# Kernel tuning notes

Measured on AMD Instinct MI355X. Metric: run time of the kernel, lower is better.

Reference implementation:

```python
import jax, jax.numpy as jnp
import numpy as np

C_IN = 128
C_INNER = 128


def setup_inputs() -> dict:
    key = jax.random.key(0)
    ks = jax.random.split(key, 9)
    b, c, h, w = 4, C_IN, 64, 64
    s = 1.0 / np.sqrt(c)
    x = jax.random.normal(ks[0], (b, c, h, w), dtype=jnp.float32)
    Wq = jax.random.normal(ks[1], (C_INNER, C_IN), dtype=jnp.float32) * s
    bq = jnp.zeros((C_INNER,), dtype=jnp.float32)
    Wk = jax.random.normal(ks[2], (C_INNER, C_IN), dtype=jnp.float32) * s
    bk = jnp.zeros((C_INNER,), dtype=jnp.float32)
    Wv = jax.random.normal(ks[3], (C_INNER, C_IN), dtype=jnp.float32) * s
    bv = jnp.zeros((C_INNER,), dtype=jnp.float32)
    Wo = jax.random.normal(ks[4], (C_IN, C_INNER), dtype=jnp.float32) * (1.0 / np.sqrt(C_INNER))
    bo = jnp.zeros((C_IN,), dtype=jnp.float32)
    return {"x": x, "Wq": Wq, "bq": bq, "Wk": Wk, "bk": bk,
            "Wv": Wv, "bv": bv, "Wo": Wo, "bo": bo}


def _conv1x1(x, W, bias):
    # x: (b,c,h,w), W: (o,c) -> (b,o,h,w)
    return jnp.einsum('oc,bchw->bohw', W, x) + bias[None, :, None, None]


def reference(x, Wq, bq, Wk, bk, Wv, bv, Wo, bo):
    b, c, h, w = x.shape
    ci = Wq.shape[0]
    n = h * w
    q = _conv1x1(x, Wq, bq).reshape(b, ci, n)          # (b, ci, n)
    k = _conv1x1(x, Wk, bk).reshape(b, ci, n)          # (b, ci, n)
    v = _conv1x1(x, Wv, bv).reshape(b, ci, n)          # (b, ci, n)
    # attn = softmax(q^T @ k) over keys
    attn = jnp.einsum('bci,bcj->bij', q, k)            # (b, n, n)
    attn = jax.nn.softmax(attn, axis=-1)
    out = jnp.einsum('bij,bcj->bci', attn, v)          # (b, ci, n)
    out = out.reshape(b, ci, h, w)
    out = _conv1x1(out, Wo, bo)
    return out + x
```

## Files before the change

### kernel.cpp

```cpp
#include <hip/hip_runtime.h>
#include <math.h>
#include <stdint.h>

#define CDIM 128
#define NTOT 4096

typedef _Float16 f16x8 __attribute__((ext_vector_type(8)));
typedef float floatx4 __attribute__((ext_vector_type(4)));

static __device__ __forceinline__ floatx4 mfma16(f16x8 a, f16x8 b, floatx4 c) {
    return __builtin_amdgcn_mfma_f32_16x16x32_f16(a, b, c, 0, 0, 0);
}
static __device__ __forceinline__ unsigned short f2h(float f) {
    _Float16 h = (_Float16)f;
    return __builtin_bit_cast(unsigned short, h);
}
static __device__ __forceinline__ float h2f(unsigned short u) {
    return (float)__builtin_bit_cast(_Float16, u);
}
static __device__ __forceinline__ f16x8 ldW8f(const float* p) {
    float4 a = *(const float4*)p;
    float4 c = *(const float4*)(p + 4);
    f16x8 r;
    r[0] = (_Float16)a.x; r[1] = (_Float16)a.y; r[2] = (_Float16)a.z; r[3] = (_Float16)a.w;
    r[4] = (_Float16)c.x; r[5] = (_Float16)c.y; r[6] = (_Float16)c.z; r[7] = (_Float16)c.w;
    return r;
}

#define SWZ(row, cc) ((((row) << 7)) + ((((cc) ^ ((row) & 15))) << 3))
#define SWZ8(row, cc) ((((row) << 6)) + ((((cc) ^ ((row) & 7))) << 3))

static __device__ __forceinline__ void gload_lds16(const void* g, void* l) {
    __builtin_amdgcn_global_load_lds(
        (const __attribute__((address_space(1))) void*)g,
        (__attribute__((address_space(3))) void*)l, 16, 0, 0);
}

__global__ __launch_bounds__(256) void qkv_proj_kernel(
    const float* __restrict__ x,
    const float* __restrict__ Wq, const float* __restrict__ Wk,
    const float* __restrict__ Wv,
    const float* __restrict__ bq, const float* __restrict__ bk,
    const float* __restrict__ bv,
    unsigned short* __restrict__ qo, unsigned short* __restrict__ ko,
    unsigned short* __restrict__ vo)
{
    __shared__ __align__(16) unsigned short Xs[16][136];

    const int t = threadIdx.x;
    const int bid = blockIdx.x;
    const int swz = ((bid & 7) << 7) | (bid >> 3);
    const int b = swz >> 8;
    const int n0 = (swz & 255) * 16;
    const int w = t >> 6, quad = (t >> 4) & 3, l15 = t & 15;

    {
        const int n = (t & 3) * 4;
        const int c = (t >> 2) * 2;
        float4 xr[2];
        #pragma unroll
        for (int j = 0; j < 2; ++j)
            xr[j] = *(const float4*)&x[((size_t)b * CDIM + c + j) * NTOT + n0 + n];
        #pragma unroll
        for (int k = 0; k < 4; ++k) {
            ushort2 u;
            u.x = f2h(((const float*)&xr[0])[k]);
            u.y = f2h(((const float*)&xr[1])[k]);
            *(ushort2*)&Xs[n + k][c] = u;
        }
    }
    __syncthreads();

    f16x8 xf[4];
    #pragma unroll
    for (int f = 0; f < 4; ++f)
        xf[f] = *(const f16x8*)&Xs[l15][f * 32 + quad * 8];

    #pragma unroll
    for (int s = 0; s < 2; ++s) {
        const float* Wm = s ? Wk : Wq;
        const float* bias = s ? bk : bq;
        unsigned short* dst = s ? ko : qo;
        #pragma unroll
        for (int ot = 0; ot < 2; ++ot) {
            const int o = w * 32 + ot * 16;
            floatx4 acc = (floatx4){0.f, 0.f, 0.f, 0.f};
            #pragma unroll
            for (int f = 0; f < 4; ++f) {
                f16x8 aW = ldW8f(&Wm[(size_t)(o + l15) * CDIM + f * 32 + quad * 8]);
                acc = mfma16(aW, xf[f], acc);
            }
            const int ob = o + quad * 4;
            ushort4 u;
            u.x = f2h(acc[0] + bias[ob + 0]);
            u.y = f2h(acc[1] + bias[ob + 1]);
            u.z = f2h(acc[2] + bias[ob + 2]);
            u.w = f2h(acc[3] + bias[ob + 3]);
            *(ushort4*)&dst[((size_t)b * NTOT + n0 + l15) * CDIM + ob] = u;
        }
    }
    {
        #pragma unroll
        for (int ot = 0; ot < 2; ++ot) {
            const int o = w * 32 + ot * 16 + l15;
            floatx4 acc = (floatx4){0.f, 0.f, 0.f, 0.f};
            #pragma unroll
            for (int f = 0; f < 4; ++f) {
                f16x8 bW = ldW8f(&Wv[(size_t)o * CDIM + f * 32 + quad * 8]);
                acc = mfma16(xf[f], bW, acc);
            }
            const float bv_ = bv[o];
            ushort4 u;
            u.x = f2h(acc[0] + bv_); u.y = f2h(acc[1] + bv_);
            u.z = f2h(acc[2] + bv_); u.w = f2h(acc[3] + bv_);
            *(ushort4*)&vo[((size_t)b * CDIM + o) * NTOT + n0 + quad * 4] = u;
        }
    }
}

__global__ __launch_bounds__(256, 2) void attn_kernel(
    const unsigned short* __restrict__ qg,
    const unsigned short* __restrict__ kg,
    const unsigned short* __restrict__ vg,
    unsigned short* __restrict__ Op,
    float* __restrict__ Ms, float* __restrict__ Ls)
{
    __shared__ __align__(16) unsigned short Kb[2][64 * 128];
    __shared__ __align__(16) unsigned short Vb[2][128 * 64];
    __shared__ __align__(16) unsigned short Ps[128 * 64];

    const int t = threadIdx.x;
    const int w = t >> 6, quad = (t >> 4) & 3, l15 = t & 15;

    const int bid = blockIdx.x;
    const int swz = ((bid & 7) << 6) | (bid >> 3);
    const int gidx = swz >> 5;
    const int b = gidx & 3;
    const int z = gidx >> 2;
    const int i0 = (swz & 31) * 128;
    const int jbase = z * 1024;
    const size_t vbase = (size_t)b * CDIM * NTOT;

    f16x8 bQ[2][4];
    #pragma unroll
    for (int nt = 0; nt < 2; ++nt) {
        const size_t qrow = ((size_t)b * NTOT + i0 + w * 32 + nt * 16 + l15) * CDIM;
        #pragma unroll
        for (int f = 0; f < 4; ++f)
            bQ[nt][f] = *(const f16x8*)&qg[qrow + f * 32 + quad * 8];
    }

    auto stageK = [&](unsigned short* Kd, int j0) {
        const size_t kbase = ((size_t)b * NTOT + j0) * CDIM;
        #pragma unroll
        for (int r = 0; r < 4; ++r) {
            const int flat = r * 256 + t;
            const int ldsoff = (r * 256 + (t & ~63)) * 8;
            const int krow = flat >> 4, kcc = flat & 15;
            gload_lds16(&kg[kbase + (size_t)krow * CDIM + ((kcc ^ (krow & 15)) << 3)],
                        &Kd[ldsoff]);
        }
    };
    auto stageV = [&](unsigned short* Vd, int j0) {
        const size_t vrow0 = vbase + j0;
        #pragma unroll
        for (int r = 0; r < 4; ++r) {
            const int flat = r * 256 + t;
            const int ldsoff = (r * 256 + (t & ~63)) * 8;
            const int vrow = flat >> 3, vcc = flat & 7;
            gload_lds16(&vg[vrow0 + (size_t)vrow * NTOT + ((vcc ^ (vrow & 7)) << 3)],
                        &Vd[ldsoff]);
        }
    };

    floatx4 accO[2][8];
    #pragma unroll
    for (int nt = 0; nt < 2; ++nt)
        #pragma unroll
        for (int dt = 0; dt < 8; ++dt) accO[nt][dt] = (floatx4){0.f, 0.f, 0.f, 0.f};
    float m_run[2] = {-INFINITY, -INFINITY};
    float l_part[2] = {0.f, 0.f};

    floatx4 accT[2][4];
    uint2 pu[2][4];
    f16x8 bP[2][2];

    auto QK = [&](const unsigned short* Kd) {
        #pragma unroll
        for (int nt = 0; nt < 2; ++nt)
            #pragma unroll
            for (int jt = 0; jt < 4; ++jt) accT[nt][jt] = (floatx4){0.f, 0.f, 0.f, 0.f};
        __builtin_amdgcn_s_setprio(1);
        #pragma unroll
        for (int jt = 0; jt < 4; ++jt)
            #pragma unroll
            for (int f = 0; f < 4; ++f) {
                f16x8 aK = *(const f16x8*)&Kd[SWZ(jt * 16 + l15, f * 4 + quad)];
                accT[0][jt] = mfma16(aK, bQ[0][f], accT[0][jt]);
                accT[1][jt] = mfma16(aK, bQ[1][f], accT[1][jt]);
            }
        __builtin_amdgcn_s_setprio(0);
    };
    auto RB = [&]() {
        #pragma unroll
        for (int nt = 0; nt < 2; ++nt) {
            const int prow = w * 32 + nt * 16 + l15;
            #pragma unroll
            for (int kb = 0; kb < 2; ++kb)
                bP[nt][kb] = *(const f16x8*)&Ps[SWZ8(prow, kb * 4 + quad)];
        }
    };
    auto PV = [&](const unsigned short* Vd) {
        __builtin_amdgcn_s_setprio(1);
        #pragma unroll
        for (int dt = 0; dt < 8; ++dt)
            #pragma unroll
            for (int kb = 0; kb < 2; ++kb) {
                f16x8 aV = *(const f16x8*)&Vd[SWZ8(dt * 16 + l15, kb * 4 + quad)];
                accO[0][dt] = mfma16(aV, bP[0][kb], accO[0][dt]);
                accO[1][dt] = mfma16(aV, bP[1][kb], accO[1][dt]);
            }
        __builtin_amdgcn_s_setprio(0);
    };
    auto SM = [&]() {
        #pragma unroll
        for (int nt = 0; nt < 2; ++nt) {
            float tm = accT[nt][0][0];
            #pragma unroll
            for (int jt = 0; jt < 4; ++jt)
                #pragma unroll
                for (int r = 0; r < 4; ++r) tm = fmaxf(tm, accT[nt][jt][r]);
            tm = fmaxf(tm, __shfl_xor(tm, 16));
            tm = fmaxf(tm, __shfl_xor(tm, 32));
            if (__ballot(tm > m_run[nt] + 8.f)) {
                const float m_new = fmaxf(m_run[nt], tm);
                const float alpha = __expf(m_run[nt] - m_new);
                m_run[nt] = m_new;
                l_part[nt] *= alpha;
                #pragma unroll
                for (int dt = 0; dt < 8; ++dt) {
                    accO[nt][dt][0] *= alpha; accO[nt][dt][1] *= alpha;
                    accO[nt][dt][2] *= alpha; accO[nt][dt][3] *= alpha;
                }
            }
            const float mcur = m_run[nt];
            float ps = 0.f;
            #pragma unroll
            for (int jt = 0; jt < 4; ++jt) {
                float p0 = __expf(accT[nt][jt][0] - mcur);
                float p1 = __expf(accT[nt][jt][1] - mcur);
                float p2 = __expf(accT[nt][jt][2] - mcur);
                float p3 = __expf(accT[nt][jt][3] - mcur);
                ps += (p0 + p1) + (p2 + p3);
                pu[nt][jt].x = __builtin_bit_cast(unsigned int,
                                   __builtin_amdgcn_cvt_pkrtz(p0, p1));
                pu[nt][jt].y = __builtin_bit_cast(unsigned int,
                                   __builtin_amdgcn_cvt_pkrtz(p2, p3));
            }
            l_part[nt] += ps;
        }
    };
    auto WP = [&]() {
        #pragma unroll
        for (int nt = 0; nt < 2; ++nt) {
            const int prow = w * 32 + nt * 16 + l15;
            #pragma unroll
            for (int jt = 0; jt < 4; ++jt)
                *(uint2*)&Ps[SWZ8(prow, 2 * jt + (quad >> 1)) + (quad & 1) * 4] =
                    pu[nt][jt];
        }
    };

    stageK(Kb[0], jbase);
    stageV(Vb[0], jbase);
    unsigned short *Kc = Kb[0], *Kn = Kb[1], *Vc = Vb[0], *Vn = Vb[1];

    asm volatile("s_waitcnt vmcnt(0) lgkmcnt(0)" ::: "memory");
    __builtin_amdgcn_s_barrier();
    stageK(Kn, jbase + 64);
    stageV(Vn, jbase + 64);
    QK(Kc);
    SM();
    WP();
    { unsigned short* tp = Kc; Kc = Kn; Kn = tp; tp = Vc; Vc = Vn; Vn = tp; }

    for (int it = 1; it <= 14; ++it) {
        asm volatile("s_waitcnt vmcnt(4) lgkmcnt(0)" ::: "memory");
        __builtin_amdgcn_s_barrier();
        RB();
        stageK(Kn, jbase + (it + 1) * 64);
        QK(Kc);
        PV(Vn);
        SM();
        asm volatile("s_waitcnt lgkmcnt(0)" ::: "memory");
        __builtin_amdgcn_s_barrier();
        stageV(Vn, jbase + (it + 1) * 64);
        WP();
        { unsigned short* tp = Kc; Kc = Kn; Kn = tp; tp = Vc; Vc = Vn; Vn = tp; }
    }

    asm volatile("s_waitcnt vmcnt(4) lgkmcnt(0)" ::: "memory");
    __builtin_amdgcn_s_barrier();
    RB();
    QK(Kc);
    PV(Vn);
    SM();
    WP();
    asm volatile("s_waitcnt vmcnt(0)" ::: "memory");
    __builtin_amdgcn_s_barrier();
    RB();
    PV(Vc);

    #pragma unroll
    for (int nt = 0; nt < 2; ++nt) {
        float lf = l_part[nt];
        lf += __shfl_xor(lf, 16);
        lf += __shfl_xor(lf, 32);
        const float inv = 1.0f / lf;
        const size_t orow =
            (((size_t)z * 4 + b) * NTOT + i0 + w * 32 + nt * 16 + l15) * CDIM;
        #pragma unroll
        for (int dt = 0; dt < 8; ++dt) {
            ushort4 u;
            u.x = f2h(accO[nt][dt][0] * inv); u.y = f2h(accO[nt][dt][1] * inv);
            u.z = f2h(accO[nt][dt][2] * inv); u.w = f2h(accO[nt][dt][3] * inv);
            *(ushort4*)&Op[orow + dt * 16 + quad * 4] = u;
        }
        if (quad == 0) {
            const int idx = (z * 4 + b) * NTOT + i0 + w * 32 + nt * 16 + l15;
            Ms[idx] = m_run[nt];
            Ls[idx] = lf;
        }
    }
}

__global__ __launch_bounds__(256) void out_proj_kernel(
    const unsigned short* __restrict__ Op,
    const float* __restrict__ Ms, const float* __restrict__ Ls,
    const float* __restrict__ Wo, const float* __restrict__ bo,
    const float* __restrict__ x, float* __restrict__ out)
{
    __shared__ __align__(16) unsigned short As[32][136];

    const int t = threadIdx.x, b = blockIdx.y, n0 = blockIdx.x * 32;
    const int zo = blockIdx.z * 64;
    const int w = t >> 6, quad = (t >> 4) & 3, l15 = t & 15;

    const size_t PER = (size_t)NTOT * 4 * CDIM;

    #pragma unroll
    for (int r = 0; r < 2; ++r) {
        int flat = r * 256 + t;
        int row = flat >> 4, c16 = (flat & 15) * 8;
        const int bn = b * NTOT + n0 + row;
        float m0 = Ms[bn], m1 = Ms[bn + 16384], m2 = Ms[bn + 32768], m3 = Ms[bn + 49152];
        float M = fmaxf(fmaxf(m0, m1), fmaxf(m2, m3));
        float w0 = Ls[bn]         * __expf(m0 - M);
        float w1 = Ls[bn + 16384] * __expf(m1 - M);
        float w2 = Ls[bn + 32768] * __expf(m2 - M);
        float w3 = Ls[bn + 49152] * __expf(m3 - M);
        const float inv = 1.0f / (w0 + w1 + w2 + w3);
        w0 *= inv; w1 *= inv; w2 *= inv; w3 *= inv;

        const size_t base = (size_t)bn * CDIM + c16;
        uint4 a0 = *(const uint4*)&Op[base];
        uint4 a1 = *(const uint4*)&Op[PER + base];
        uint4 a2 = *(const uint4*)&Op[2 * PER + base];
        uint4 a3 = *(const uint4*)&Op[3 * PER + base];
        const unsigned short* p0 = (const unsigned short*)&a0;
        const unsigned short* p1 = (const unsigned short*)&a1;
        const unsigned short* p2 = (const unsigned short*)&a2;
        const unsigned short* p3 = (const unsigned short*)&a3;
        unsigned short mv[8];
        #pragma unroll
        for (int j = 0; j < 8; ++j)
            mv[j] = f2h(w0 * h2f(p0[j]) + w1 * h2f(p1[j]) +
                        w2 * h2f(p2[j]) + w3 * h2f(p3[j]));
        *(uint4*)&As[row][c16] = *(const uint4*)mv;
    }
    __syncthreads();

    const int nt = w & 1, oh = w >> 1;
    f16x8 bA[4];
    #pragma unroll
    for (int f = 0; f < 4; ++f)
        bA[f] = *(const f16x8*)&As[nt * 16 + l15][f * 32 + quad * 8];

    #pragma unroll
    for (int ot = 0; ot < 2; ++ot) {
        const int o = zo + oh * 32 + ot * 16;
        floatx4 acc = (floatx4){0.f, 0.f, 0.f, 0.f};
        #pragma unroll
        for (int f = 0; f < 4; ++f) {
            f16x8 aW = ldW8f(&Wo[(size_t)(o + l15) * CDIM + f * 32 + quad * 8]);
            acc = mfma16(aW, bA[f], acc);
        }
        const int ob = o + quad * 4;
        #pragma unroll
        for (int r = 0; r < 4; ++r) {
            size_t idx = ((size_t)b * CDIM + ob + r) * NTOT + n0 + nt * 16 + l15;
            out[idx] = acc[r] + bo[ob + r] + x[idx];
        }
    }
}

extern "C" void kernel_launch(void* const* d_in, const int* in_sizes, int n_in,
                              void* d_out, int out_size, void* d_ws, size_t ws_size,
                              hipStream_t stream)
{
    const float* x  = (const float*)d_in[0];
    const float* Wq = (const float*)d_in[1];
    const float* bq = (const float*)d_in[2];
    const float* Wk = (const float*)d_in[3];
    const float* bk = (const float*)d_in[4];
    const float* Wv = (const float*)d_in[5];
    const float* bv = (const float*)d_in[6];
    const float* Wo = (const float*)d_in[7];
    const float* bo = (const float*)d_in[8];
    float* out = (float*)d_out;

    const size_t PER = (size_t)4 * CDIM * NTOT;
    unsigned short* q_ws  = (unsigned short*)d_ws;
    unsigned short* k_ws  = q_ws + PER;
    unsigned short* v_ws  = k_ws + PER;
    unsigned short* op_ws = v_ws + PER;
    float*          ms_ws = (float*)(op_ws + 4 * PER);
    float*          ls_ws = ms_ws + 4 * 16384;

    qkv_proj_kernel<<<dim3(1024), dim3(256), 0, stream>>>(
        x, Wq, Wk, Wv, bq, bk, bv, q_ws, k_ws, v_ws);
    attn_kernel<<<dim3(512), dim3(256), 0, stream>>>(
        q_ws, k_ws, v_ws, op_ws, ms_ws, ls_ws);
    out_proj_kernel<<<dim3(128, 4, 2), dim3(256), 0, stream>>>(
        op_ws, ms_ws, ls_ws, Wo, bo, x, out);
}
```

Measured before the change: 159.1 us.

## Stage projection weights in LDS and enlarge pixel tiles in proj kernels

The QKV and output projection kernels now convert each block's weight slice to fp16 once and keep it in shared memory. Before, every wave re-read fp32 weights from global memory and converted them per MFMA fragment. Tiles grow to 64 pixels per block, and the QKV kernel splits output channels across two z-blocks. This reuses weights across more pixels at the cost of more LDS per block and a second read of x in the QKV kernel.

Measured after the change: 140.4 us. -11.8%, faster.

```diff
diff --git a/kernel.cpp b/kernel.cpp
--- a/kernel.cpp
+++ b/kernel.cpp
@@ -17,14 +17,6 @@
 }
 static __device__ __forceinline__ float h2f(unsigned short u) {
     return (float)__builtin_bit_cast(_Float16, u);
-}
-static __device__ __forceinline__ f16x8 ldW8f(const float* p) {
-    float4 a = *(const float4*)p;
-    float4 c = *(const float4*)(p + 4);
-    f16x8 r;
-    r[0] = (_Float16)a.x; r[1] = (_Float16)a.y; r[2] = (_Float16)a.z; r[3] = (_Float16)a.w;
-    r[4] = (_Float16)c.x; r[5] = (_Float16)c.y; r[6] = (_Float16)c.z; r[7] = (_Float16)c.w;
-    return r;
 }
 
 #define SWZ(row, cc) ((((row) << 7)) + ((((cc) ^ ((row) & 15))) << 3))
@@ -45,28 +37,46 @@
     unsigned short* __restrict__ qo, unsigned short* __restrict__ ko,
     unsigned short* __restrict__ vo)
 {
-    __shared__ __align__(16) unsigned short Xs[16][136];
-
-    const int t = threadIdx.x;
-    const int bid = blockIdx.x;
-    const int swz = ((bid & 7) << 7) | (bid >> 3);
-    const int b = swz >> 8;
-    const int n0 = (swz & 255) * 16;
+    __shared__ __align__(16) unsigned short Xs[64][136];
+    __shared__ __align__(16) unsigned short Ws[3][64][136];
+
+    const int t = threadIdx.x, b = blockIdx.y, n0 = blockIdx.x * 64;
+    const int zo = blockIdx.z * 64;
     const int w = t >> 6, quad = (t >> 4) & 3, l15 = t & 15;
 
     {
-        const int n = (t & 3) * 4;
-        const int c = (t >> 2) * 2;
-        float4 xr[2];
-        #pragma unroll
-        for (int j = 0; j < 2; ++j)
+        const int n = (t & 15) * 4;
+        const int c = (t >> 4) * 8;
+        float4 xr[8];
+        #pragma unroll
+        for (int j = 0; j < 8; ++j)
             xr[j] = *(const float4*)&x[((size_t)b * CDIM + c + j) * NTOT + n0 + n];
         #pragma unroll
         for (int k = 0; k < 4; ++k) {
-            ushort2 u;
-            u.x = f2h(((const float*)&xr[0])[k]);
-            u.y = f2h(((const float*)&xr[1])[k]);
-            *(ushort2*)&Xs[n + k][c] = u;
+            ushort4 ulo, uhi;
+            ulo.x = f2h(((const float*)&xr[0])[k]);
+            ulo.y = f2h(((const float*)&xr[1])[k]);
+            ulo.z = f2h(((const float*)&xr[2])[k]);
+            ulo.w = f2h(((const float*)&xr[3])[k]);
+            uhi.x = f2h(((const float*)&xr[4])[k]);
+            uhi.y = f2h(((const float*)&xr[5])[k]);
+            uhi.z = f2h(((const float*)&xr[6])[k]);
+            uhi.w = f2h(((const float*)&xr[7])[k]);
+            *(ushort4*)&Xs[n + k][c]     = ulo;
+            *(ushort4*)&Xs[n + k][c + 4] = uhi;
+        }
+    }
+    {
+        const int o = t >> 2, ch = (t & 3) * 32;
+        #pragma unroll
+        for (int s = 0; s < 3; ++s) {
+            const float* W = (s == 0) ? Wq : (s == 1) ? Wk : Wv;
+            #pragma unroll
+            for (int i = 0; i < 8; ++i) {
+                float4 f4 = *(const float4*)&W[(size_t)(zo + o) * CDIM + ch + i * 4];
+                ushort4 u = { f2h(f4.x), f2h(f4.y), f2h(f4.z), f2h(f4.w) };
+                *(ushort4*)&Ws[s][o][ch + i * 4] = u;
+            }
         }
     }
     __syncthreads();
@@ -74,47 +84,43 @@
     f16x8 xf[4];
     #pragma unroll
     for (int f = 0; f < 4; ++f)
-        xf[f] = *(const f16x8*)&Xs[l15][f * 32 + quad * 8];
+        xf[f] = *(const f16x8*)&Xs[w * 16 + l15][f * 32 + quad * 8];
 
     #pragma unroll
     for (int s = 0; s < 2; ++s) {
-        const float* Wm = s ? Wk : Wq;
         const float* bias = s ? bk : bq;
         unsigned short* dst = s ? ko : qo;
         #pragma unroll
-        for (int ot = 0; ot < 2; ++ot) {
-            const int o = w * 32 + ot * 16;
+        for (int ot = 0; ot < 4; ++ot) {
             floatx4 acc = (floatx4){0.f, 0.f, 0.f, 0.f};
             #pragma unroll
             for (int f = 0; f < 4; ++f) {
-                f16x8 aW = ldW8f(&Wm[(size_t)(o + l15) * CDIM + f * 32 + quad * 8]);
+                f16x8 aW = *(const f16x8*)&Ws[s][ot * 16 + l15][f * 32 + quad * 8];
                 acc = mfma16(aW, xf[f], acc);
             }
-            const int ob = o + quad * 4;
+            const int ob = zo + ot * 16 + quad * 4;
             ushort4 u;
             u.x = f2h(acc[0] + bias[ob + 0]);
             u.y = f2h(acc[1] + bias[ob + 1]);
             u.z = f2h(acc[2] + bias[ob + 2]);
             u.w = f2h(acc[3] + bias[ob + 3]);
-            *(ushort4*)&dst[((size_t)b * NTOT + n0 + l15) * CDIM + ob] = u;
-        }
-    }
-    {
-        #pragma unroll
-        for (int ot = 0; ot < 2; ++ot) {
-            const int o = w * 32 + ot * 16 + l15;
-            floatx4 acc = (floatx4){0.f, 0.f, 0.f, 0.f};
-            #pragma unroll
-            for (int f = 0; f < 4; ++f) {
-                f16x8 bW = ldW8f(&Wv[(size_t)o * CDIM + f * 32 + quad * 8]);
-                acc = mfma16(xf[f], bW, acc);
-            }
-            const float bv_ = bv[o];
-            ushort4 u;
-            u.x = f2h(acc[0] + bv_); u.y = f2h(acc[1] + bv_);
-            u.z = f2h(acc[2] + bv_); u.w = f2h(acc[3] + bv_);
-            *(ushort4*)&vo[((size_t)b * CDIM + o) * NTOT + n0 + quad * 4] = u;
-        }
+            *(ushort4*)&dst[((size_t)b * NTOT + n0 + w * 16 + l15) * CDIM + ob] = u;
+        }
+    }
+    #pragma unroll
+    for (int ot = 0; ot < 4; ++ot) {
+        floatx4 acc = (floatx4){0.f, 0.f, 0.f, 0.f};
+        #pragma unroll
+        for (int f = 0; f < 4; ++f) {
+            f16x8 bW = *(const f16x8*)&Ws[2][ot * 16 + l15][f * 32 + quad * 8];
+            acc = mfma16(xf[f], bW, acc);
+        }
+        const int o = zo + ot * 16 + l15;
+        const float bv_ = bv[o];
+        ushort4 u;
+        u.x = f2h(acc[0] + bv_); u.y = f2h(acc[1] + bv_);
+        u.z = f2h(acc[2] + bv_); u.w = f2h(acc[3] + bv_);
+        *(ushort4*)&vo[((size_t)b * CDIM + o) * NTOT + n0 + w * 16 + quad * 4] = u;
     }
 }
 
@@ -340,16 +346,17 @@
     const float* __restrict__ Wo, const float* __restrict__ bo,
     const float* __restrict__ x, float* __restrict__ out)
 {
-    __shared__ __align__(16) unsigned short As[32][136];
-
-    const int t = threadIdx.x, b = blockIdx.y, n0 = blockIdx.x * 32;
+    __shared__ __align__(16) unsigned short As[64][136];
+    __shared__ __align__(16) unsigned short Ws[64][136];
+
+    const int t = threadIdx.x, b = blockIdx.y, n0 = blockIdx.x * 64;
     const int zo = blockIdx.z * 64;
     const int w = t >> 6, quad = (t >> 4) & 3, l15 = t & 15;
 
     const size_t PER = (size_t)NTOT * 4 * CDIM;
 
     #pragma unroll
-    for (int r = 0; r < 2; ++r) {
+    for (int r = 0; r < 4; ++r) {
         int flat = r * 256 + t;
         int row = flat >> 4, c16 = (flat & 15) * 8;
         const int bn = b * NTOT + n0 + row;
@@ -378,27 +385,34 @@
                         w2 * h2f(p2[j]) + w3 * h2f(p3[j]));
         *(uint4*)&As[row][c16] = *(const uint4*)mv;
     }
+    {
+        int o = t >> 2, ch = (t & 3) * 32;
+        #pragma unroll
+        for (int i = 0; i < 8; ++i) {
+            float4 f4 = *(const float4*)&Wo[(size_t)(zo + o) * CDIM + ch + i * 4];
+            ushort4 u = { f2h(f4.x), f2h(f4.y), f2h(f4.z), f2h(f4.w) };
+            *(ushort4*)&Ws[o][ch + i * 4] = u;
+        }
+    }
     __syncthreads();
 
-    const int nt = w & 1, oh = w >> 1;
     f16x8 bA[4];
     #pragma unroll
     for (int f = 0; f < 4; ++f)
-        bA[f] = *(const f16x8*)&As[nt * 16 + l15][f * 32 + quad * 8];
-
-    #pragma unroll
-    for (int ot = 0; ot < 2; ++ot) {
-        const int o = zo + oh * 32 + ot * 16;
+        bA[f] = *(const f16x8*)&As[w * 16 + l15][f * 32 + quad * 8];
+
+    #pragma unroll
+    for (int ot = 0; ot < 4; ++ot) {
         floatx4 acc = (floatx4){0.f, 0.f, 0.f, 0.f};
         #pragma unroll
         for (int f = 0; f < 4; ++f) {
-            f16x8 aW = ldW8f(&Wo[(size_t)(o + l15) * CDIM + f * 32 + quad * 8]);
+            f16x8 aW = *(const f16x8*)&Ws[ot * 16 + l15][f * 32 + quad * 8];
             acc = mfma16(aW, bA[f], acc);
         }
-        const int ob = o + quad * 4;
+        const int ob = zo + ot * 16 + quad * 4;
         #pragma unroll
         for (int r = 0; r < 4; ++r) {
-            size_t idx = ((size_t)b * CDIM + ob + r) * NTOT + n0 + nt * 16 + l15;
+            size_t idx = ((size_t)b * CDIM + ob + r) * NTOT + n0 + w * 16 + l15;
             out[idx] = acc[r] + bo[ob + r] + x[idx];
         }
     }
@@ -427,10 +441,10 @@
     float*          ms_ws = (float*)(op_ws + 4 * PER);
     float*          ls_ws = ms_ws + 4 * 16384;
 
-    qkv_proj_kernel<<<dim3(1024), dim3(256), 0, stream>>>(
+    qkv_proj_kernel<<<dim3(64, 4, 2), dim3(256), 0, stream>>>(
         x, Wq, Wk, Wv, bq, bk, bv, q_ws, k_ws, v_ws);
     attn_kernel<<<dim3(512), dim3(256), 0, stream>>>(
         q_ws, k_ws, v_ws, op_ws, ms_ws, ls_ws);
-    out_proj_kernel<<<dim3(128, 4, 2), dim3(256), 0, stream>>>(
+    out_proj_kernel<<<dim3(64, 4, 2), dim3(256), 0, stream>>>(
         op_ws, ms_ws, ls_ws, Wo, bo, x, out);
 }
```
